# Kernel tuning notes

Measured on AMD Instinct MI355X. Metric: run time of the kernel, lower is better.

The kernel has to match this reference:

```python
import jax, jax.numpy as jnp
import numpy as np

N = 100000
E = 3200000
F_IN = 512
H = 16
C = 40


def gcn_conv(x, edge_index, W, b, num_nodes):
    """PyG GCNConv: y = D^{-1/2} (A + I) D^{-1/2} (x @ W) + b.
    edge_index: [2, E] int, row=source, col=target; self-loops added here."""
    # transform first (small hidden dim keeps message traffic low)
    h = x @ W  # [N, out]
    loops = jnp.arange(num_nodes, dtype=edge_index.dtype)
    row = jnp.concatenate([edge_index[0], loops])
    col = jnp.concatenate([edge_index[1], loops])
    deg = jax.ops.segment_sum(jnp.ones_like(col, dtype=h.dtype), col,
                              num_segments=num_nodes)  # in-degree incl. self-loop
    dinv = jnp.where(deg > 0, jax.lax.rsqrt(deg), 0.0)
    norm = dinv[row] * dinv[col]  # [E+N]
    msgs = h[row] * norm[:, None]  # gather + scale, [E+N, out]
    out = jax.ops.segment_sum(msgs, col, num_segments=num_nodes)  # scatter-add
    return out + b


def setup_inputs() -> dict:
    key = jax.random.key(0)
    k1, k2, k3, k4, k5, k6 = jax.random.split(key, 6)
    x = jax.random.normal(k1, (N, F_IN), dtype=jnp.float32)
    edge_index = jax.random.randint(k2, (2, E), 0, N, dtype=jnp.int64)
    s1 = 1.0 / np.sqrt(F_IN)
    s2 = 1.0 / np.sqrt(H)
    W1 = jax.random.uniform(k3, (F_IN, H), jnp.float32, -s1, s1)
    b1 = jnp.zeros((H,), jnp.float32)
    W2 = jax.random.uniform(k4, (H, C), jnp.float32, -s2, s2)
    b2 = jnp.zeros((C,), jnp.float32)
    return {"x": x, "edge_index": edge_index, "W1": W1, "b1": b1,
            "W2": W2, "b2": b2}


def reference(x, edge_index, W1, b1, W2, b2):
    h = gcn_conv(x, edge_index, W1, b1, N)
    h = jax.nn.relu(h)
    # F.dropout(training=self.training): inference mode -> identity
    h = gcn_conv(h, edge_index, W2, b2, N)
    return jax.nn.log_softmax(h, axis=1)
```

## Files before the change

kernel.cpp:

```cpp
#include <hip/hip_runtime.h>

#define NN 100000
#define EE 3200000
#define FIN 512
#define HH 16
#define CC 40

#define SHIFT 9
#define BNODES 512
#define NB 196
#define CAP 20480
#define CH 2048
#define TC ((EE + CH - 1) / CH)
#define GB ((NN * 4 + 255) / 256)

__device__ __forceinline__ float bf2f(unsigned short u) {
    return __uint_as_float(((unsigned)u) << 16);
}
__device__ __forceinline__ unsigned short f2bf(float f) {
    unsigned b = __float_as_uint(f);
    return (unsigned short)((b + 0x7FFF + ((b >> 16) & 1)) >> 16);
}

__global__ void k_bin(const int* __restrict__ ei, int* __restrict__ head,
                      unsigned* __restrict__ pairs) {
    __shared__ int h[NB];
    __shared__ int gbase[NB];
    __shared__ int lhead[NB];
    __shared__ unsigned esrc[CH];
    __shared__ unsigned edst[CH];
    __shared__ int is64_s;
    int t = threadIdx.x;
    if (t < 64) {
        int nz = (ei[2 * t + 1] != 0) ? 1 : 0;
        unsigned long long m = __ballot(nz);
        if (t == 0) is64_s = (m == 0ULL) ? 1 : 0;
    }
    for (int i = t; i < NB; i += 256) { h[i] = 0; lhead[i] = 0; }
    __syncthreads();
    int is64 = is64_s;
    int e0 = blockIdx.x * CH, e1 = min(EE, e0 + CH);
    for (int e = e0 + t; e < e1; e += 256) {
        int src = is64 ? ei[2 * e] : ei[e];
        int dst = is64 ? ei[2 * (EE + e)] : ei[EE + e];
        esrc[e - e0] = (unsigned)src;
        edst[e - e0] = (unsigned)dst;
        atomicAdd(&h[dst >> SHIFT], 1);
    }
    __syncthreads();
    for (int i = t; i < NB; i += 256)
        gbase[i] = h[i] ? atomicAdd(&head[i], h[i]) : 0;
    __syncthreads();
    int n = e1 - e0;
    for (int j = t; j < n; j += 256) {
        unsigned src = esrc[j];
        unsigned dst = edst[j];
        int b = (int)(dst >> SHIFT);
        int p = gbase[b] + atomicAdd(&lhead[b], 1);
        pairs[(size_t)b * CAP + p] = ((dst & (BNODES - 1)) << 17) | src;
    }
}

__global__ void __launch_bounds__(256) k_buildgemm(
        const unsigned* __restrict__ pairs, const int* __restrict__ head,
        int* __restrict__ ptr, int* __restrict__ pend,
        float* __restrict__ dinv, int* __restrict__ srcs,
        const float* __restrict__ x, const float* __restrict__ W1,
        float* __restrict__ g1f) {
    __shared__ float w1s[FIN * HH];
    int t = threadIdx.x;
    if (blockIdx.x < NB) {
        int* h   = (int*)w1s;
        int* lex = (int*)w1s + BNODES;
        int* ws  = (int*)w1s + 2 * BNODES;
        int b = blockIdx.x, lane = t & 63, wid = t >> 6;
        int node0 = b << SHIFT;
        int p0 = b * CAP;
        int cnt = head[b];
        for (int i = t; i < BNODES; i += 256) h[i] = 0;
        __syncthreads();
        for (int p = t; p < cnt; p += 256) atomicAdd(&h[pairs[p0 + p] >> 17], 1);
        __syncthreads();
        int a0 = h[2 * t], a1 = h[2 * t + 1];
        int s = a0 + a1;
        int v = s;
#pragma unroll
        for (int off = 1; off < 64; off <<= 1) {
            int u = __shfl_up(v, off);
            if (lane >= off) v += u;
        }
        if (lane == 63) ws[wid] = v;
        __syncthreads();
        int add = 0;
        for (int w = 0; w < wid; ++w) add += ws[w];
        int incl = v + add;
        int e0 = incl - s;
        lex[2 * t] = e0;
        lex[2 * t + 1] = e0 + a0;
        __syncthreads();
        for (int i = t; i < BNODES; i += 256) {
            int n = node0 + i;
            if (n < NN) {
                int st = p0 + lex[i];
                ptr[n] = st;
                pend[n] = st + h[i];
                dinv[n] = rsqrtf((float)(h[i] + 1));
            }
        }
        __syncthreads();
        for (int p = t; p < cnt; p += 256) {
            unsigned w = pairs[p0 + p];
            int pos = p0 + atomicAdd(&lex[w >> 17], 1);
            srcs[pos] = (int)(w & 0x1FFFF);
        }
    } else {
        for (int i = t; i < FIN * HH; i += 256) w1s[i] = W1[i];
        __syncthreads();
        int gt = (blockIdx.x - NB) * 256 + t;
        int node = gt >> 2, q = gt & 3;
        if (node >= NN) return;
        const float4* xr = reinterpret_cast<const float4*>(x + (size_t)node * FIN + q * 128);
        float acc[HH];
#pragma unroll
        for (int f = 0; f < HH; ++f) acc[f] = 0.f;
#pragma unroll 4
        for (int kq = 0; kq < 32; ++kq) {
            float4 xv = xr[kq];
            const float* wr = w1s + (q * 128 + kq * 4) * HH;
#pragma unroll
            for (int f = 0; f < HH; ++f) acc[f] = fmaf(xv.x, wr[f], acc[f]);
#pragma unroll
            for (int f = 0; f < HH; ++f) acc[f] = fmaf(xv.y, wr[HH + f], acc[f]);
#pragma unroll
            for (int f = 0; f < HH; ++f) acc[f] = fmaf(xv.z, wr[2 * HH + f], acc[f]);
#pragma unroll
            for (int f = 0; f < HH; ++f) acc[f] = fmaf(xv.w, wr[3 * HH + f], acc[f]);
        }
#pragma unroll
        for (int f = 0; f < HH; ++f) {
            acc[f] += __shfl_xor(acc[f], 1);
            acc[f] += __shfl_xor(acc[f], 2);
        }
        float4 o = make_float4(acc[4 * q + 0], acc[4 * q + 1],
                               acc[4 * q + 2], acc[4 * q + 3]);
        reinterpret_cast<float4*>(g1f)[node * 4 + q] = o;
    }
}

__global__ void k_scale(const float* __restrict__ g1f, const float* __restrict__ dinv,
                        unsigned short* __restrict__ g1) {
    int gt = blockIdx.x * 256 + threadIdx.x;
    int node = gt >> 2, q = gt & 3;
    if (node >= NN) return;
    float di = dinv[node];
    float4 v = reinterpret_cast<const float4*>(g1f)[node * 4 + q];
    ushort4 o;
    o.x = f2bf(v.x * di);
    o.y = f2bf(v.y * di);
    o.z = f2bf(v.z * di);
    o.w = f2bf(v.w * di);
    reinterpret_cast<ushort4*>(g1)[node * 4 + q] = o;
}

__global__ void k_agg1(const unsigned short* __restrict__ g1, const int* __restrict__ ptr,
                       const int* __restrict__ pend, const int* __restrict__ srcs,
                       const float* __restrict__ dinv, const float* __restrict__ b1,
                       unsigned short* __restrict__ g2h) {
    int gt = blockIdx.x * blockDim.x + threadIdx.x;
    int node = gt >> 2, q = gt & 3;
    if (node >= NN) return;
    const ushort4* G = reinterpret_cast<const ushort4*>(g1);
    ushort4 sv = G[node * 4 + q];
    float ax = bf2f(sv.x), ay = bf2f(sv.y), az = bf2f(sv.z), aw = bf2f(sv.w);
    float bx = 0.f, by = 0.f, bz = 0.f, bw = 0.f;
    float cx = 0.f, cy = 0.f, cz = 0.f, cw = 0.f;
    float dx = 0.f, dy = 0.f, dz = 0.f, dw = 0.f;
    int e = ptr[node], e1 = pend[node];
    for (; e + 3 < e1; e += 4) {
        int s0 = srcs[e], s1 = srcs[e + 1], s2 = srcs[e + 2], s3 = srcs[e + 3];
        ushort4 v0 = G[s0 * 4 + q];
        ushort4 v1 = G[s1 * 4 + q];
        ushort4 v2 = G[s2 * 4 + q];
        ushort4 v3 = G[s3 * 4 + q];
        ax += bf2f(v0.x); ay += bf2f(v0.y); az += bf2f(v0.z); aw += bf2f(v0.w);
        bx += bf2f(v1.x); by += bf2f(v1.y); bz += bf2f(v1.z); bw += bf2f(v1.w);
        cx += bf2f(v2.x); cy += bf2f(v2.y); cz += bf2f(v2.z); cw += bf2f(v2.w);
        dx += bf2f(v3.x); dy += bf2f(v3.y); dz += bf2f(v3.z); dw += bf2f(v3.w);
    }
    for (; e < e1; ++e) {
        ushort4 v = G[srcs[e] * 4 + q];
        ax += bf2f(v.x); ay += bf2f(v.y); az += bf2f(v.z); aw += bf2f(v.w);
    }
    ax += bx + cx + dx;
    ay += by + cy + dy;
    az += bz + cz + dz;
    aw += bw + cw + dw;
    float di = dinv[node];
    const float4 bb = reinterpret_cast<const float4*>(b1)[q];
    ushort4 r;
    r.x = f2bf(fmaxf(fmaf(di, ax, bb.x), 0.f) * di);
    r.y = f2bf(fmaxf(fmaf(di, ay, bb.y), 0.f) * di);
    r.z = f2bf(fmaxf(fmaf(di, az, bb.z), 0.f) * di);
    r.w = f2bf(fmaxf(fmaf(di, aw, bb.w), 0.f) * di);
    reinterpret_cast<ushort4*>(g2h)[node * 4 + q] = r;
}

__global__ void __launch_bounds__(256) k_agg2out(
        const unsigned short* __restrict__ g2h, const int* __restrict__ ptr,
        const int* __restrict__ pend, const int* __restrict__ srcs,
        const float* __restrict__ dinv, const float* __restrict__ W2,
        const float* __restrict__ b2, float* __restrict__ out) {
    __shared__ float w2s[HH * 41];
    __shared__ float b2s[CC];
    int t = threadIdx.x;
    for (int i = t; i < HH * CC; i += 256) w2s[(i / CC) * 41 + (i % CC)] = W2[i];
    if (t < CC) b2s[t] = b2[t];
    __syncthreads();
    int gt = blockIdx.x * blockDim.x + t;
    int node = gt >> 2, q = gt & 3;
    if (node >= NN) return;
    const ushort4* G = reinterpret_cast<const ushort4*>(g2h);
    ushort4 sv = G[node * 4 + q];
    float ax = bf2f(sv.x), ay = bf2f(sv.y), az = bf2f(sv.z), aw = bf2f(sv.w);
    float bx = 0.f, by = 0.f, bz = 0.f, bw = 0.f;
    float cx = 0.f, cy = 0.f, cz = 0.f, cw = 0.f;
    float dx = 0.f, dy = 0.f, dz = 0.f, dw = 0.f;
    int e = ptr[node], e1 = pend[node];
    for (; e + 3 < e1; e += 4) {
        int s0 = srcs[e], s1 = srcs[e + 1], s2 = srcs[e + 2], s3 = srcs[e + 3];
        ushort4 v0 = G[s0 * 4 + q];
        ushort4 v1 = G[s1 * 4 + q];
        ushort4 v2 = G[s2 * 4 + q];
        ushort4 v3 = G[s3 * 4 + q];
        ax += bf2f(v0.x); ay += bf2f(v0.y); az += bf2f(v0.z); aw += bf2f(v0.w);
        bx += bf2f(v1.x); by += bf2f(v1.y); bz += bf2f(v1.z); bw += bf2f(v1.w);
        cx += bf2f(v2.x); cy += bf2f(v2.y); cz += bf2f(v2.z); cw += bf2f(v2.w);
        dx += bf2f(v3.x); dy += bf2f(v3.y); dz += bf2f(v3.z); dw += bf2f(v3.w);
    }
    for (; e < e1; ++e) {
        ushort4 v = G[srcs[e] * 4 + q];
        ax += bf2f(v.x); ay += bf2f(v.y); az += bf2f(v.z); aw += bf2f(v.w);
    }
    ax += bx + cx + dx;
    ay += by + cy + dy;
    az += bz + cz + dz;
    aw += bw + cw + dw;
    const float* w0 = w2s + (4 * q + 0) * 41;
    const float* w1 = w2s + (4 * q + 1) * 41;
    const float* w2r = w2s + (4 * q + 2) * 41;
    const float* w3 = w2s + (4 * q + 3) * 41;
    float y[CC];
#pragma unroll
    for (int c = 0; c < CC; ++c)
        y[c] = fmaf(ax, w0[c], fmaf(ay, w1[c], fmaf(az, w2r[c], aw * w3[c])));
#pragma unroll
    for (int c = 0; c < CC; ++c) {
        y[c] += __shfl_xor(y[c], 1);
        y[c] += __shfl_xor(y[c], 2);
    }
    float di = dinv[node];
    float m = -3.0e38f;
#pragma unroll
    for (int c = 0; c < CC; ++c) {
        y[c] = fmaf(di, y[c], b2s[c]);
        m = fmaxf(m, y[c]);
    }
    float ssum = 0.f;
#pragma unroll
    for (int c = 0; c < CC; ++c) ssum += expf(y[c] - m);
    float l = logf(ssum) + m;
    float ov[10];
#pragma unroll
    for (int c = 0; c < CC; ++c) {
        if ((c / 10) == q) ov[c % 10] = y[c] - l;
    }
    float2* o2 = reinterpret_cast<float2*>(out + (size_t)node * CC + 10 * q);
#pragma unroll
    for (int i = 0; i < 5; ++i) o2[i] = make_float2(ov[2 * i], ov[2 * i + 1]);
}

extern "C" void kernel_launch(void* const* d_in, const int* in_sizes, int n_in,
                              void* d_out, int out_size, void* d_ws, size_t ws_size,
                              hipStream_t stream) {
    const float* x  = (const float*)d_in[0];
    const int*   ei = (const int*)d_in[1];
    const float* W1 = (const float*)d_in[2];
    const float* b1 = (const float*)d_in[3];
    const float* W2 = (const float*)d_in[4];
    const float* b2 = (const float*)d_in[5];
    float* out = (float*)d_out;

    char* w = (char*)d_ws;
    auto alloc = [&](size_t bytes) {
        char* p = w;
        w += (bytes + 255) & ~(size_t)255;
        return p;
    };
    int*            head  = (int*)alloc((size_t)NB * 4);
    int*            ptr   = (int*)alloc((size_t)NN * 4);
    int*            pend  = (int*)alloc((size_t)NN * 4);
    float*          dinv  = (float*)alloc((size_t)NN * 4);
    unsigned*       pairs = (unsigned*)alloc((size_t)NB * CAP * 4);
    int*            srcs  = (int*)alloc((size_t)NB * CAP * 4);
    float*          g1f   = (float*)alloc((size_t)NN * HH * 4);
    unsigned short* g1    = (unsigned short*)alloc((size_t)NN * HH * 2);
    unsigned short* g2h   = (unsigned short*)alloc((size_t)NN * HH * 2);

    hipMemsetAsync(head, 0, (size_t)NB * sizeof(int), stream);
    k_bin<<<TC, 256, 0, stream>>>(ei, head, pairs);
    k_buildgemm<<<NB + GB, 256, 0, stream>>>(pairs, head, ptr, pend, dinv, srcs,
                                             x, W1, g1f);
    k_scale<<<GB, 256, 0, stream>>>(g1f, dinv, g1);
    int nt = NN * 4;
    k_agg1<<<(nt + 255) / 256, 256, 0, stream>>>(g1, ptr, pend, srcs, dinv, b1, g2h);
    k_agg2out<<<(nt + 255) / 256, 256, 0, stream>>>(g2h, ptr, pend, srcs, dinv,
                                                    W2, b2, out);
}
```

Baseline: 470.1 us.

## Fuse degree scaling into the GEMM by computing degree via global atomics in binning

Per-node in-degree is now counted with global atomics during edge binning, so the dense x@W1 blocks can apply the D^-1/2 scaling and bf16 conversion directly. This removes the separate scale kernel and the fp32 intermediate buffer. The GEMM is restructured so each block handles 64 nodes with four wave-uniform K slices, reading W1 straight from global memory with scalar loads instead of staging it in LDS, and reducing the partial sums through padded shared memory. The cost is 3.2M extra global atomics in k_bin and a larger memset.

```diff
diff --git a/kernel.cpp b/kernel.cpp
--- a/kernel.cpp
+++ b/kernel.cpp
@@ -12,7 +12,7 @@
 #define CAP 20480
 #define CH 2048
 #define TC ((EE + CH - 1) / CH)
-#define GB ((NN * 4 + 255) / 256)
+#define GB2 ((NN + 63) / 64)
 
 __device__ __forceinline__ float bf2f(unsigned short u) {
     return __uint_as_float(((unsigned)u) << 16);
@@ -23,7 +23,7 @@
 }
 
 __global__ void k_bin(const int* __restrict__ ei, int* __restrict__ head,
-                      unsigned* __restrict__ pairs) {
+                      int* __restrict__ deg, unsigned* __restrict__ pairs) {
     __shared__ int h[NB];
     __shared__ int gbase[NB];
     __shared__ int lhead[NB];
@@ -46,6 +46,7 @@
         esrc[e - e0] = (unsigned)src;
         edst[e - e0] = (unsigned)dst;
         atomicAdd(&h[dst >> SHIFT], 1);
+        atomicAdd(&deg[dst], 1);
     }
     __syncthreads();
     for (int i = t; i < NB; i += 256)
@@ -66,13 +67,13 @@
         int* __restrict__ ptr, int* __restrict__ pend,
         float* __restrict__ dinv, int* __restrict__ srcs,
         const float* __restrict__ x, const float* __restrict__ W1,
-        float* __restrict__ g1f) {
-    __shared__ float w1s[FIN * HH];
+        const int* __restrict__ deg, unsigned short* __restrict__ g1) {
+    __shared__ float red[4][64][17];
     int t = threadIdx.x;
     if (blockIdx.x < NB) {
-        int* h   = (int*)w1s;
-        int* lex = (int*)w1s + BNODES;
-        int* ws  = (int*)w1s + 2 * BNODES;
+        int* h   = (int*)red;
+        int* lex = (int*)red + BNODES;
+        int* wsm = (int*)red + 2 * BNODES;
         int b = blockIdx.x, lane = t & 63, wid = t >> 6;
         int node0 = b << SHIFT;
         int p0 = b * CAP;
@@ -89,10 +90,10 @@
             int u = __shfl_up(v, off);
             if (lane >= off) v += u;
         }
-        if (lane == 63) ws[wid] = v;
+        if (lane == 63) wsm[wid] = v;
         __syncthreads();
         int add = 0;
-        for (int w = 0; w < wid; ++w) add += ws[w];
+        for (int w = 0; w < wid; ++w) add += wsm[w];
         int incl = v + add;
         int e0 = incl - s;
         lex[2 * t] = e0;
@@ -114,19 +115,20 @@
             srcs[pos] = (int)(w & 0x1FFFF);
         }
     } else {
-        for (int i = t; i < FIN * HH; i += 256) w1s[i] = W1[i];
-        __syncthreads();
-        int gt = (blockIdx.x - NB) * 256 + t;
-        int node = gt >> 2, q = gt & 3;
-        if (node >= NN) return;
-        const float4* xr = reinterpret_cast<const float4*>(x + (size_t)node * FIN + q * 128);
+        int kq = __builtin_amdgcn_readfirstlane(t >> 6);
+        int n = t & 63;
+        int base = (blockIdx.x - NB) * 64;
+        int nc = min(base + n, NN - 1);
+        const float4* xr = reinterpret_cast<const float4*>(
+            x + (size_t)nc * FIN + kq * 128);
+        const float* wb = W1 + kq * 128 * HH;
         float acc[HH];
 #pragma unroll
         for (int f = 0; f < HH; ++f) acc[f] = 0.f;
-#pragma unroll 4
-        for (int kq = 0; kq < 32; ++kq) {
-            float4 xv = xr[kq];
-            const float* wr = w1s + (q * 128 + kq * 4) * HH;
+#pragma unroll 2
+        for (int i = 0; i < 32; ++i) {
+            float4 xv = xr[i];
+            const float* wr = wb + i * 4 * HH;
 #pragma unroll
             for (int f = 0; f < HH; ++f) acc[f] = fmaf(xv.x, wr[f], acc[f]);
 #pragma unroll
@@ -137,29 +139,25 @@
             for (int f = 0; f < HH; ++f) acc[f] = fmaf(xv.w, wr[3 * HH + f], acc[f]);
         }
 #pragma unroll
-        for (int f = 0; f < HH; ++f) {
-            acc[f] += __shfl_xor(acc[f], 1);
-            acc[f] += __shfl_xor(acc[f], 2);
-        }
-        float4 o = make_float4(acc[4 * q + 0], acc[4 * q + 1],
-                               acc[4 * q + 2], acc[4 * q + 3]);
-        reinterpret_cast<float4*>(g1f)[node * 4 + q] = o;
-    }
-}
-
-__global__ void k_scale(const float* __restrict__ g1f, const float* __restrict__ dinv,
-                        unsigned short* __restrict__ g1) {
-    int gt = blockIdx.x * 256 + threadIdx.x;
-    int node = gt >> 2, q = gt & 3;
-    if (node >= NN) return;
-    float di = dinv[node];
-    float4 v = reinterpret_cast<const float4*>(g1f)[node * 4 + q];
-    ushort4 o;
-    o.x = f2bf(v.x * di);
-    o.y = f2bf(v.y * di);
-    o.z = f2bf(v.z * di);
-    o.w = f2bf(v.w * di);
-    reinterpret_cast<ushort4*>(g1)[node * 4 + q] = o;
+        for (int f = 0; f < HH; ++f) red[kq][n][f] = acc[f];
+        __syncthreads();
+        int g = t >> 6;
+        int f0 = g * 4;
+        float r0 = red[0][n][f0]     + red[1][n][f0]     + red[2][n][f0]     + red[3][n][f0];
+        float r1 = red[0][n][f0 + 1] + red[1][n][f0 + 1] + red[2][n][f0 + 1] + red[3][n][f0 + 1];
+        float r2 = red[0][n][f0 + 2] + red[1][n][f0 + 2] + red[2][n][f0 + 2] + red[3][n][f0 + 2];
+        float r3 = red[0][n][f0 + 3] + red[1][n][f0 + 3] + red[2][n][f0 + 3] + red[3][n][f0 + 3];
+        int node = base + n;
+        if (node < NN) {
+            float di = rsqrtf((float)(deg[node] + 1));
+            ushort4 o;
+            o.x = f2bf(r0 * di);
+            o.y = f2bf(r1 * di);
+            o.z = f2bf(r2 * di);
+            o.w = f2bf(r3 * di);
+            reinterpret_cast<ushort4*>(g1)[node * 4 + g] = o;
+        }
+    }
 }
 
 __global__ void k_agg1(const unsigned short* __restrict__ g1, const int* __restrict__ ptr,
@@ -296,21 +294,20 @@
         w += (bytes + 255) & ~(size_t)255;
         return p;
     };
-    int*            head  = (int*)alloc((size_t)NB * 4);
+    int*            head  = (int*)alloc((size_t)(NB + NN) * 4);
+    int*            deg   = head + NB;
     int*            ptr   = (int*)alloc((size_t)NN * 4);
     int*            pend  = (int*)alloc((size_t)NN * 4);
     float*          dinv  = (float*)alloc((size_t)NN * 4);
     unsigned*       pairs = (unsigned*)alloc((size_t)NB * CAP * 4);
     int*            srcs  = (int*)alloc((size_t)NB * CAP * 4);
-    float*          g1f   = (float*)alloc((size_t)NN * HH * 4);
     unsigned short* g1    = (unsigned short*)alloc((size_t)NN * HH * 2);
     unsigned short* g2h   = (unsigned short*)alloc((size_t)NN * HH * 2);
 
-    hipMemsetAsync(head, 0, (size_t)NB * sizeof(int), stream);
-    k_bin<<<TC, 256, 0, stream>>>(ei, head, pairs);
-    k_buildgemm<<<NB + GB, 256, 0, stream>>>(pairs, head, ptr, pend, dinv, srcs,
-                                             x, W1, g1f);
-    k_scale<<<GB, 256, 0, stream>>>(g1f, dinv, g1);
+    hipMemsetAsync(head, 0, (size_t)(NB + NN) * sizeof(int), stream);
+    k_bin<<<TC, 256, 0, stream>>>(ei, head, deg, pairs);
+    k_buildgemm<<<NB + GB2, 256, 0, stream>>>(pairs, head, ptr, pend, dinv, srcs,
+                                              x, W1, deg, g1);
     int nt = NN * 4;
     k_agg1<<<(nt + 255) / 256, 256, 0, stream>>>(g1, ptr, pend, srcs, dinv, b1, g2h);
     k_agg2out<<<(nt + 255) / 256, 256, 0, stream>>>(g2h, ptr, pend, srcs, dinv,
```

New measurement: 570.6 us. 1.21x slower.
